# Optimization experiments

Hardware: AMD Instinct MI355X
Metric: run time of the kernel (lower is better)

## Reference

```python
import jax, jax.numpy as jnp
import numpy as np
from jax import lax

NUM_BASIS = 2048
SHAPE = (32, 32)
DIM_BASIS = SHAPE[0] * SHAPE[1]
BATCH = 8192
LAM = 0.1          # l1 sparsity penalty (typical sparse-coding default)
N_ITER = 100       # FISTA iterations
N_POWER = 50       # power-iteration steps for Lipschitz constant


def _soft(z, thr):
    return jnp.sign(z) * jnp.maximum(jnp.abs(z) - thr, 0.0)


def _fista(x, phi):
    """x: [B, D], phi: [K, D] (detached) -> alpha: [B, K]."""
    G = phi @ phi.T  # [K, K] Gram matrix
    # Lipschitz constant L = lambda_max(G) via power iteration
    v = jnp.ones((G.shape[0],), G.dtype)
    def piter(v, _):
        w = G @ v
        return w / jnp.linalg.norm(w), None
    v, _ = lax.scan(piter, v, None, length=N_POWER)
    L = v @ (G @ v)  # Rayleigh quotient
    step = 1.0 / L
    thr = LAM * step

    B, K = x.shape[0], phi.shape[0]
    alpha0 = jnp.zeros((B, K), x.dtype)
    t0 = jnp.asarray(1.0, x.dtype)

    def body(carry, _):
        alpha_prev, y, t = carry
        grad = (y @ phi - x) @ phi.T            # [B,K]
        alpha = _soft(y - step * grad, thr)     # prox step
        t_new = 0.5 * (1.0 + jnp.sqrt(1.0 + 4.0 * t * t))
        y_new = alpha + ((t - 1.0) / t_new) * (alpha - alpha_prev)
        return (alpha, y_new, t_new), None

    (alpha, _, _), _ = lax.scan(body, (alpha0, alpha0, t0), None, length=N_ITER)
    return alpha


def reference(x, phi):
    # x: [B, H, W] -> flatten to [B, D]
    xf = x.reshape(x.shape[0], -1)
    # solver uses detached phi (phi.detach() in the torch code; inference
    # of alpha is treated as non-differentiable, as in the original repo)
    alpha = _fista(lax.stop_gradient(xf), lax.stop_gradient(phi))
    recon = (alpha @ phi).reshape(-1, SHAPE[0], SHAPE[1])
    return alpha, recon


def setup_inputs() -> dict:
    key = jax.random.key(0)
    kx, kp = jax.random.split(key)
    x = jax.random.normal(kx, (BATCH, SHAPE[0], SHAPE[1]), dtype=jnp.float32)
    phi = jax.random.normal(kp, (NUM_BASIS, DIM_BASIS), dtype=jnp.float32)
    phi = phi / jnp.linalg.norm(phi, axis=1, keepdims=True)  # F.normalize(p=2, dim=1)
    return {"x": x, "phi": phi}
```

## Files before the change

### kernel.cpp

```cpp
#include <hip/hip_runtime.h>
#include <math.h>

#define BATCH 8192
#define KB 2048
#define DD 1024
#define LAM 0.1f
#define N_ITER 100
#define N_POWER 50
#define NTILES 32

typedef unsigned short u16;
using short8 = __attribute__((ext_vector_type(8))) short;
using f32x4  = __attribute__((ext_vector_type(4))) float;

__device__ __forceinline__ u16 f2bf(float f) {
  unsigned int u = __builtin_bit_cast(unsigned int, f);
  u = u + 0x7FFFu + ((u >> 16) & 1u);
  return (u16)(u >> 16);
}
__device__ __forceinline__ float bf2f(u16 s) {
  unsigned int u = ((unsigned int)s) << 16;
  return __builtin_bit_cast(float, u);
}

__device__ __forceinline__ u16 f2h(float f) {
  _Float16 h = (_Float16)f;
  return __builtin_bit_cast(unsigned short, h);
}
__device__ __forceinline__ float h2f(u16 s) {
  _Float16 h = __builtin_bit_cast(_Float16, s);
  return (float)h;
}

__global__ void k_split_f32(const float* __restrict__ in, u16* __restrict__ h,
                            u16* __restrict__ lo, int n) {
  for (int i = blockIdx.x * blockDim.x + threadIdx.x; i < n; i += gridDim.x * blockDim.x) {
    float v = in[i];
    u16 hh = f2bf(v);
    h[i] = hh;
    lo[i] = f2bf(v - bf2f(hh));
  }
}

__global__ __launch_bounds__(256) void k_split_phiT(const float* __restrict__ phi,
                                                    u16* __restrict__ th, u16* __restrict__ tl) {
  __shared__ float t[32][33];
  int k0 = blockIdx.y * 32, d0 = blockIdx.x * 32;
  int tx = threadIdx.x & 31, ty = threadIdx.x >> 5;
#pragma unroll
  for (int rr = 0; rr < 32; rr += 8)
    t[ty + rr][tx] = phi[(size_t)(k0 + ty + rr) * DD + d0 + tx];
  __syncthreads();
#pragma unroll
  for (int rr = 0; rr < 32; rr += 8) {
    float v = t[tx][ty + rr];
    u16 hh = f2bf(v);
    size_t idx = (size_t)(d0 + ty + rr) * KB + (k0 + tx);
    th[idx] = hh;
    tl[idx] = f2bf(v - bf2f(hh));
  }
}

__global__ void k_cvt_f16(const float* __restrict__ in, u16* __restrict__ h, int n) {
  for (int i = blockIdx.x * blockDim.x + threadIdx.x; i < n; i += gridDim.x * blockDim.x)
    h[i] = f2h(in[i]);
}

__global__ void k_init_pw(float* __restrict__ w, float* __restrict__ pA) {
  int i = blockIdx.x * 256 + threadIdx.x;
  if (i < KB) w[i] = 1.f;
  if (i < 64) pA[i] = 1.f / 64.f;
}

template <int MODE>
__global__ __launch_bounds__(256) void k_power_fused(const float* __restrict__ G,
                                                     const float* __restrict__ win,
                                                     float* __restrict__ wout,
                                                     const float* __restrict__ pin,
                                                     float* __restrict__ pout) {
  int rloc = threadIdx.x >> 3;
  int seg = threadIdx.x & 7;
  int row = blockIdx.x * 32 + rloc;
  float n2 = 0.f;
#pragma unroll
  for (int i = 0; i < 64; ++i) n2 += pin[i];
  float n = sqrtf(n2);
  const float* g = G + (size_t)row * KB + seg * 256;
  const float* vv = win + seg * 256;
  float s = 0.f;
#pragma unroll 8
  for (int j = 0; j < 256; j += 4) {
    float4 gg = *(const float4*)(g + j);
    float4 vx = *(const float4*)(vv + j);
    s = fmaf(gg.x, vx.x, fmaf(gg.y, vx.y, fmaf(gg.z, vx.z, fmaf(gg.w, vx.w, s))));
  }
#pragma unroll
  for (int off = 1; off < 8; off <<= 1) s += __shfl_xor(s, off, 64);
  s = s / n;
  float val;
  if (MODE == 0) {
    if (seg == 0) wout[row] = s;
    val = (seg == 0) ? s * s : 0.f;
  } else {
    val = (seg == 0) ? (win[row] / n) * s : 0.f;
  }
#pragma unroll
  for (int off = 8; off < 64; off <<= 1) val += __shfl_xor(val, off, 64);
  __shared__ float red[4];
  int lane = threadIdx.x & 63, wid = threadIdx.x >> 6;
  if (lane == 0) red[wid] = val;
  __syncthreads();
  if (threadIdx.x == 0) pout[blockIdx.x] = red[0] + red[1] + red[2] + red[3];
}

__global__ void k_compute_step(const float* __restrict__ partialL, float* __restrict__ stepbuf) {
  float L = 0.f;
#pragma unroll
  for (int i = 0; i < 64; ++i) L += partialL[i];
  stepbuf[0] = 1.f / L;
}

template <int EPI>
__global__ __launch_bounds__(256) void k_xphiT(
    const u16* __restrict__ Ah, const u16* __restrict__ Al,
    const u16* __restrict__ Bh, const u16* __restrict__ Bl,
    u16* __restrict__ out16, float* __restrict__ out32, int N, int K) {
  __shared__ u16 lds[4 * 128 * 32];
  const int tid = threadIdx.x;
  const int w = tid >> 6, l = tid & 63;
  const int row0 = blockIdx.y * 128, col0 = blockIdx.x * 128;
  const int wm = (w >> 1) * 64, wn = (w & 1) * 64;
  const int lrow = l & 15, lk = (l >> 4) * 8;

  f32x4 zero4 = {0.f, 0.f, 0.f, 0.f};
  f32x4 acc[4][4];
#pragma unroll
  for (int i = 0; i < 4; ++i)
#pragma unroll
    for (int j = 0; j < 4; ++j) acc[i][j] = zero4;

  for (int k0 = 0; k0 < K; k0 += 32) {
    {
      const u16* gs[4] = {Ah, Al, Bh, Bl};
      const int r0s[4] = {row0, row0, col0, col0};
#pragma unroll
      for (int st = 0; st < 4; ++st) {
        u16* s = lds + st * 4096;
#pragma unroll
        for (int h = 0; h < 2; ++h) {
          int ch = h * 256 + w * 64 + l;
          const u16* gp = gs[st] + (size_t)(r0s[st] + (ch >> 2)) * K + k0 + (ch & 3) * 8;
          u16* sp = s + (h * 256 + w * 64) * 8;
          __builtin_amdgcn_global_load_lds((const __attribute__((address_space(1))) void*)gp,
                                           (__attribute__((address_space(3))) void*)sp, 16, 0, 0);
        }
      }
    }
    __syncthreads();
    short8 ah[4], al[4];
#pragma unroll
    for (int i = 0; i < 4; ++i) {
      int r = wm + i * 16 + lrow;
      ah[i] = *(const short8*)&lds[0 * 4096 + r * 32 + lk];
      al[i] = *(const short8*)&lds[1 * 4096 + r * 32 + lk];
    }
#pragma unroll
    for (int j = 0; j < 4; ++j) {
      int r = wn + j * 16 + lrow;
      short8 bh = *(const short8*)&lds[2 * 4096 + r * 32 + lk];
      short8 bl = *(const short8*)&lds[3 * 4096 + r * 32 + lk];
#pragma unroll
      for (int i = 0; i < 4; ++i) {
        acc[i][j] = __builtin_amdgcn_mfma_f32_16x16x32_bf16(ah[i], bh, acc[i][j], 0, 0, 0);
        acc[i][j] = __builtin_amdgcn_mfma_f32_16x16x32_bf16(ah[i], bl, acc[i][j], 0, 0, 0);
        acc[i][j] = __builtin_amdgcn_mfma_f32_16x16x32_bf16(al[i], bh, acc[i][j], 0, 0, 0);
      }
    }
    __syncthreads();
  }
#pragma unroll
  for (int i = 0; i < 4; ++i)
#pragma unroll
    for (int r = 0; r < 4; ++r) {
      int m = row0 + wm + i * 16 + ((l >> 4) << 2) + r;
      size_t base = (size_t)m * N;
#pragma unroll
      for (int j = 0; j < 4; ++j) {
        int n = col0 + wn + j * 16 + (l & 15);
        float v = acc[i][j][r];
        if (EPI == 0) {
          out16[base + n] = f2h(v);
        } else {
          out32[base + n] = v;
        }
      }
    }
}

__global__ void k_iter0(const u16* __restrict__ Cx, u16* __restrict__ Yout,
                        u16* __restrict__ Af16, const float* __restrict__ stepbuf) {
  const float step = stepbuf[0];
  const float thr = LAM * step;
  int n = BATCH * KB;
  for (int i = blockIdx.x * blockDim.x + threadIdx.x; i < n; i += gridDim.x * blockDim.x) {
    float z = step * h2f(Cx[i]);
    float az = fabsf(z) - thr;
    float a = az > 0.f ? copysignf(az, z) : 0.f;
    u16 ah = f2h(a);
    Af16[i] = ah;
    Yout[i] = ah;
  }
}


__device__ __forceinline__ void stage_op(const u16* src, int r0, int q0,
                                         u16* ldsbase, int tid) {
#pragma unroll
  for (int i = 0; i < 4; ++i) {
    int c = i * 512 + tid;
    int r = c >> 3;
    int sp = (c & 7) ^ (r & 7);
    const u16* gp = src + ((size_t)(r0 + r) << 11) + (q0 + (sp << 3));
    u16* lp = ldsbase + ((i * 512 + (tid & 448)) << 3);
    __builtin_amdgcn_global_load_lds((const __attribute__((address_space(1))) void*)gp,
                                     (__attribute__((address_space(3))) void*)lp, 16, 0, 0);
  }
}

__global__ __launch_bounds__(512, 1) void k_fista_fused(
    const u16* __restrict__ Yin, u16* __restrict__ Yout, u16* Af16,
    const u16* __restrict__ Gh,
    const u16* __restrict__ Cx, float* AlphaOut,
    const float* __restrict__ stepbuf, float mu, int last) {
  __shared__ u16 lds[65536];

  const int tid = threadIdx.x;
  const int w = tid >> 6, l = tid & 63;
  const int wm = w >> 2, wn = w & 3;
  const int lr = l & 15, lg = l >> 4;

  const int lin = blockIdx.x + (int)gridDim.x * blockIdx.y;
  const int bq = lin >> 6;
  const int bp = (lin >> 3) & 7;
  const int br = lin & 7;
  const int row0 = ((bq << 3) + br) * 256;
  const int col0 = bp * 256;

  f32x4 acc[8][4];
  f32x4 zero4 = {0.f, 0.f, 0.f, 0.f};
#pragma unroll
  for (int i = 0; i < 8; ++i)
#pragma unroll
    for (int j = 0; j < 4; ++j) acc[i][j] = zero4;

  stage_op(Yin, row0, 0, lds, tid);
  stage_op(Gh, col0, 0, lds + 16384, tid);

#define FBODY(TT, B)                                                              \
  {                                                                               \
    asm volatile("s_waitcnt vmcnt(0)" ::: "memory");                              \
    __builtin_amdgcn_s_barrier();                                                 \
    __builtin_amdgcn_sched_barrier(0);                                            \
    {                                                                             \
      int tn = (TT) + 1;                                                          \
      if (tn >= NTILES) tn = 0;                                                   \
      int q0 = tn << 6;                                                           \
      stage_op(Yin, row0, q0, lds + ((B) ? 0 : 32768), tid);                      \
      stage_op(Gh, col0, q0, lds + ((B) ? 0 : 32768) + 16384, tid);               \
    }                                                                             \
    __builtin_amdgcn_sched_barrier(0);                                            \
    const u16* baseA = lds + ((B) ? 32768 : 0);                                   \
    const u16* baseB = baseA + 16384;                                             \
    short8 bf[4][2];                                                              \
    _Pragma("unroll") for (int j = 0; j < 4; ++j) {                               \
      _Pragma("unroll") for (int ks = 0; ks < 2; ++ks) {                          \
        int brow = wn * 64 + j * 16 + lr;                                         \
        int slot = ks * 4 + lg;                                                   \
        bf[j][ks] = *(const short8*)(baseB + brow * 64 + ((slot ^ (brow & 7)) << 3)); \
      }                                                                           \
    }                                                                             \
    __builtin_amdgcn_s_setprio(1);                                                \
    _Pragma("unroll") for (int i = 0; i < 8; ++i) {                               \
      int arow = wm * 128 + i * 16 + lr;                                          \
      short8 a0 = *(const short8*)(baseA + arow * 64 + (((0 + lg) ^ (arow & 7)) << 3)); \
      short8 a1 = *(const short8*)(baseA + arow * 64 + (((4 + lg) ^ (arow & 7)) << 3)); \
      _Pragma("unroll") for (int j = 0; j < 4; ++j) {                             \
        acc[i][j] = __builtin_amdgcn_mfma_f32_16x16x32_f16(a0, bf[j][0], acc[i][j], 0, 0, 0); \
        acc[i][j] = __builtin_amdgcn_mfma_f32_16x16x32_f16(a1, bf[j][1], acc[i][j], 0, 0, 0); \
      }                                                                           \
    }                                                                             \
    __builtin_amdgcn_s_setprio(0);                                                \
  }

  for (int tt = 0; tt < NTILES; tt += 2) {
    FBODY(tt, 0)
    FBODY(tt + 1, 1)
  }
#undef FBODY

  const float step = stepbuf[0];
  const float thr = LAM * step;
#pragma unroll
  for (int i = 0; i < 8; ++i) {
#pragma unroll
    for (int r = 0; r < 4; ++r) {
      int m = row0 + wm * 128 + i * 16 + (lg << 2) + r;
      size_t base = (size_t)m * KB;
#pragma unroll
      for (int j = 0; j < 4; ++j) {
        int n = col0 + wn * 64 + j * 16 + lr;
        size_t idx = base + n;
        float g = acc[i][j][r] - h2f(Cx[idx]);
        float y = h2f(Yin[idx]);
        float z = y - step * g;
        float az = fabsf(z) - thr;
        float a = az > 0.f ? copysignf(az, z) : 0.f;
        float ap = h2f(Af16[idx]);
        float yn = a + mu * (a - ap);
        Af16[idx] = f2h(a);
        if (last) AlphaOut[idx] = a;
        Yout[idx] = f2h(yn);
      }
    }
  }
}

extern "C" void kernel_launch(void* const* d_in, const int* in_sizes, int n_in,
                              void* d_out, int out_size, void* d_ws, size_t ws_size,
                              hipStream_t stream) {
  const float* x = (const float*)d_in[0];
  const float* phi = (const float*)d_in[1];
  float* out = (float*)d_out;
  float* alpha = out;
  float* reconF = out + (size_t)BATCH * KB;

  char* ws = (char*)d_ws;
  u16* YA = (u16*)ws;
  u16* Af16 = (u16*)(ws + 33554432ull);
  u16* Gph = (u16*)(ws + 67108864ull);
  u16* Gpl = (u16*)(ws + 75497472ull);
  u16* Cx16 = (u16*)(ws + 83886080ull);
  float* Gf = (float*)(ws + 117440512ull);
  float* stepbuf = (float*)(ws + 150994944ull);
  const size_t need = 150995008ull;
  if (ws_size < need) return;

  u16* YB = (u16*)reconF;

  u16* xh = (u16*)reconF;
  u16* xl = xh + (size_t)BATCH * DD;
  float* vA = reconF;
  float* vB = reconF + 2048;
  float* pA = reconF + 4096;
  float* pB = reconF + 4224;

  k_split_f32<<<2048, 256, 0, stream>>>(phi, Gph, Gpl, KB * DD);
  k_split_f32<<<2048, 256, 0, stream>>>(x, xh, xl, BATCH * DD);

  k_xphiT<0><<<dim3(KB / 128, BATCH / 128), 256, 0, stream>>>(
      xh, xl, Gph, Gpl, Cx16, nullptr, KB, DD);

  k_xphiT<1><<<dim3(KB / 128, KB / 128), 256, 0, stream>>>(
      Gph, Gpl, Gph, Gpl, nullptr, Gf, KB, DD);

  k_init_pw<<<8, 256, 0, stream>>>(vA, pA);
  for (int s = 0; s < N_POWER; ++s) {
    const float* win = (s & 1) ? vB : vA;
    float* wout = (s & 1) ? vA : vB;
    const float* pin = (s & 1) ? pB : pA;
    float* pout = (s & 1) ? pA : pB;
    k_power_fused<0><<<64, 256, 0, stream>>>(Gf, win, wout, pin, pout);
  }
  k_power_fused<1><<<64, 256, 0, stream>>>(Gf, vA, nullptr, pA, pB);
  k_compute_step<<<1, 1, 0, stream>>>(pB, stepbuf);

  k_cvt_f16<<<2048, 256, 0, stream>>>(Gf, Gph, KB * KB);

  k_iter0<<<2048, 256, 0, stream>>>(Cx16, YA, Af16, stepbuf);

  float t = 1.f;
  float mus[N_ITER];
  for (int it = 0; it < N_ITER; ++it) {
    float tn = 0.5f * (1.f + sqrtf(1.f + 4.f * t * t));
    mus[it] = (t - 1.f) / tn;
    t = tn;
  }
  u16* ycur = YA;
  u16* ynext = YB;
  for (int it = 1; it < N_ITER; ++it) {
    int last = (it == N_ITER - 1) ? 1 : 0;
    k_fista_fused<<<dim3(KB / 256, BATCH / 256), 512, 0, stream>>>(
        ycur, ynext, Af16, Gph, Cx16, alpha, stepbuf, mus[it], last);
    u16* tmp = ycur; ycur = ynext; ynext = tmp;
  }

  u16* aH = YA;
  u16* aL = Af16;
  u16* pTh = (u16*)Gf;
  u16* pTl = pTh + (size_t)DD * KB;
  k_split_f32<<<2048, 256, 0, stream>>>(alpha, aH, aL, BATCH * KB);
  k_split_phiT<<<dim3(DD / 32, KB / 32), 256, 0, stream>>>(phi, pTh, pTl);
  k_xphiT<1><<<dim3(DD / 128, BATCH / 128), 256, 0, stream>>>(
      aH, aL, pTh, pTl, nullptr, reconF, DD, KB);
}
```

Before: 10.00 ms.

## Replace double-buffered 256x256 FISTA GEMM with simple 128x128 single-buffer tiles

Rewrites the fused FISTA iteration kernel to use 128x128 output tiles with 256 threads, a K-step of 32, and a single LDS buffer synchronised by two barriers per step. This replaces the earlier 256x256 tile with swizzled, double-buffered async staging. The smaller LDS footprint lets more blocks run per CU, but it loses load/compute overlap, reduces operand reuse per loaded byte, and drops the bank-conflict swizzle. The grid remapping keeps an L2-friendly block ordering.

Measured after the change: 14.20 ms. 1.42x slower.

```diff
diff --git a/kernel.cpp b/kernel.cpp
--- a/kernel.cpp
+++ b/kernel.cpp
@@ -7,7 +7,6 @@
 #define LAM 0.1f
 #define N_ITER 100
 #define N_POWER 50
-#define NTILES 32
 
 typedef unsigned short u16;
 using short8 = __attribute__((ext_vector_type(8))) short;
@@ -213,102 +212,80 @@
 }
 
 
-__device__ __forceinline__ void stage_op(const u16* src, int r0, int q0,
-                                         u16* ldsbase, int tid) {
-#pragma unroll
-  for (int i = 0; i < 4; ++i) {
-    int c = i * 512 + tid;
-    int r = c >> 3;
-    int sp = (c & 7) ^ (r & 7);
-    const u16* gp = src + ((size_t)(r0 + r) << 11) + (q0 + (sp << 3));
-    u16* lp = ldsbase + ((i * 512 + (tid & 448)) << 3);
-    __builtin_amdgcn_global_load_lds((const __attribute__((address_space(1))) void*)gp,
-                                     (__attribute__((address_space(3))) void*)lp, 16, 0, 0);
-  }
-}
-
-__global__ __launch_bounds__(512, 1) void k_fista_fused(
+__global__ __launch_bounds__(256) void k_fista_fused(
     const u16* __restrict__ Yin, u16* __restrict__ Yout, u16* Af16,
     const u16* __restrict__ Gh,
     const u16* __restrict__ Cx, float* AlphaOut,
     const float* __restrict__ stepbuf, float mu, int last) {
-  __shared__ u16 lds[65536];
+  __shared__ u16 lds[2 * 128 * 32];
 
   const int tid = threadIdx.x;
   const int w = tid >> 6, l = tid & 63;
-  const int wm = w >> 2, wn = w & 3;
-  const int lr = l & 15, lg = l >> 4;
-
-  const int lin = blockIdx.x + (int)gridDim.x * blockIdx.y;
-  const int bq = lin >> 6;
-  const int bp = (lin >> 3) & 7;
-  const int br = lin & 7;
-  const int row0 = ((bq << 3) + br) * 256;
-  const int col0 = bp * 256;
-
-  f32x4 acc[8][4];
+  const int wm = (w >> 1) * 64, wn = (w & 1) * 64;
+  const int lrow = l & 15, lk = (l >> 4) * 8;
+
+  const int lin = blockIdx.x;
+  const int by = ((lin >> 7) << 3) + (lin & 7);
+  const int bx = (lin >> 3) & 15;
+  const int row0 = by * 128, col0 = bx * 128;
+
   f32x4 zero4 = {0.f, 0.f, 0.f, 0.f};
-#pragma unroll
-  for (int i = 0; i < 8; ++i)
+  f32x4 acc[4][4];
+#pragma unroll
+  for (int i = 0; i < 4; ++i)
 #pragma unroll
     for (int j = 0; j < 4; ++j) acc[i][j] = zero4;
 
-  stage_op(Yin, row0, 0, lds, tid);
-  stage_op(Gh, col0, 0, lds + 16384, tid);
-
-#define FBODY(TT, B)                                                              \
-  {                                                                               \
-    asm volatile("s_waitcnt vmcnt(0)" ::: "memory");                              \
-    __builtin_amdgcn_s_barrier();                                                 \
-    __builtin_amdgcn_sched_barrier(0);                                            \
-    {                                                                             \
-      int tn = (TT) + 1;                                                          \
-      if (tn >= NTILES) tn = 0;                                                   \
-      int q0 = tn << 6;                                                           \
-      stage_op(Yin, row0, q0, lds + ((B) ? 0 : 32768), tid);                      \
-      stage_op(Gh, col0, q0, lds + ((B) ? 0 : 32768) + 16384, tid);               \
-    }                                                                             \
-    __builtin_amdgcn_sched_barrier(0);                                            \
-    const u16* baseA = lds + ((B) ? 32768 : 0);                                   \
-    const u16* baseB = baseA + 16384;                                             \
-    short8 bf[4][2];                                                              \
-    _Pragma("unroll") for (int j = 0; j < 4; ++j) {                               \
-      _Pragma("unroll") for (int ks = 0; ks < 2; ++ks) {                          \
-        int brow = wn * 64 + j * 16 + lr;                                         \
-        int slot = ks * 4 + lg;                                                   \
-        bf[j][ks] = *(const short8*)(baseB + brow * 64 + ((slot ^ (brow & 7)) << 3)); \
-      }                                                                           \
-    }                                                                             \
-    __builtin_amdgcn_s_setprio(1);                                                \
-    _Pragma("unroll") for (int i = 0; i < 8; ++i) {                               \
-      int arow = wm * 128 + i * 16 + lr;                                          \
-      short8 a0 = *(const short8*)(baseA + arow * 64 + (((0 + lg) ^ (arow & 7)) << 3)); \
-      short8 a1 = *(const short8*)(baseA + arow * 64 + (((4 + lg) ^ (arow & 7)) << 3)); \
-      _Pragma("unroll") for (int j = 0; j < 4; ++j) {                             \
-        acc[i][j] = __builtin_amdgcn_mfma_f32_16x16x32_f16(a0, bf[j][0], acc[i][j], 0, 0, 0); \
-        acc[i][j] = __builtin_amdgcn_mfma_f32_16x16x32_f16(a1, bf[j][1], acc[i][j], 0, 0, 0); \
-      }                                                                           \
-    }                                                                             \
-    __builtin_amdgcn_s_setprio(0);                                                \
-  }
-
-  for (int tt = 0; tt < NTILES; tt += 2) {
-    FBODY(tt, 0)
-    FBODY(tt + 1, 1)
-  }
-#undef FBODY
+  for (int k0 = 0; k0 < KB; k0 += 32) {
+    {
+      const u16* gs[2] = {Yin, Gh};
+      const int r0s[2] = {row0, col0};
+#pragma unroll
+      for (int st = 0; st < 2; ++st) {
+        u16* s = lds + st * 4096;
+#pragma unroll
+        for (int h = 0; h < 2; ++h) {
+          int ch = h * 256 + w * 64 + l;
+          const u16* gp = gs[st] + (size_t)(r0s[st] + (ch >> 2)) * KB + k0 + (ch & 3) * 8;
+          u16* sp = s + (h * 256 + w * 64) * 8;
+          __builtin_amdgcn_global_load_lds((const __attribute__((address_space(1))) void*)gp,
+                                           (__attribute__((address_space(3))) void*)sp, 16, 0, 0);
+        }
+      }
+    }
+    __syncthreads();
+    short8 af[4], bf[4];
+#pragma unroll
+    for (int i = 0; i < 4; ++i) {
+      int r = wm + i * 16 + lrow;
+      af[i] = *(const short8*)&lds[0 * 4096 + r * 32 + lk];
+    }
+#pragma unroll
+    for (int j = 0; j < 4; ++j) {
+      int r = wn + j * 16 + lrow;
+      bf[j] = *(const short8*)&lds[1 * 4096 + r * 32 + lk];
+    }
+    __builtin_amdgcn_s_setprio(1);
+#pragma unroll
+    for (int i = 0; i < 4; ++i)
+#pragma unroll
+      for (int j = 0; j < 4; ++j)
+        acc[i][j] = __builtin_amdgcn_mfma_f32_16x16x32_f16(af[i], bf[j], acc[i][j], 0, 0, 0);
+    __builtin_amdgcn_s_setprio(0);
+    __syncthreads();
+  }
 
   const float step = stepbuf[0];
   const float thr = LAM * step;
 #pragma unroll
-  for (int i = 0; i < 8; ++i) {
+  for (int i = 0; i < 4; ++i) {
 #pragma unroll
     for (int r = 0; r < 4; ++r) {
-      int m = row0 + wm * 128 + i * 16 + (lg << 2) + r;
+      int m = row0 + wm + i * 16 + ((l >> 4) << 2) + r;
       size_t base = (size_t)m * KB;
 #pragma unroll
       for (int j = 0; j < 4; ++j) {
-        int n = col0 + wn * 64 + j * 16 + lr;
+        int n = col0 + wn + j * 16 + (l & 15);
         size_t idx = base + n;
         float g = acc[i][j][r] - h2f(Cx[idx]);
         float y = h2f(Yin[idx]);
@@ -389,7 +366,7 @@
   u16* ynext = YB;
   for (int it = 1; it < N_ITER; ++it) {
     int last = (it == N_ITER - 1) ? 1 : 0;
-    k_fista_fused<<<dim3(KB / 256, BATCH / 256), 512, 0, stream>>>(
+    k_fista_fused<<<dim3(1024), 256, 0, stream>>>(
         ycur, ynext, Af16, Gph, Cx16, alpha, stepbuf, mus[it], last);
     u16* tmp = ycur; ycur = ynext; ynext = tmp;
   }
```
